# Performance work log

Hardware: AMD Instinct MI355X
Metric: run time of the kernel (lower is better)

## Reference

```python
import jax, jax.numpy as jnp
import numpy as np

B, T, U = 4, 256, 128
EH, PH, JH, V = 1024, 640, 640, 1024


def setup_inputs() -> dict:
    key = jax.random.key(0)
    ks = jax.random.split(key, 8)
    s_e = 1.0 / np.sqrt(EH)
    s_p = 1.0 / np.sqrt(PH)
    s_j = 1.0 / np.sqrt(JH)
    return {
        "enc": jax.random.normal(ks[0], (B, EH, T), jnp.float32),
        "dec": jax.random.normal(ks[1], (B, PH, U), jnp.float32),
        "W_enc": jax.random.uniform(ks[2], (JH, EH), jnp.float32, -s_e, s_e),
        "b_enc": jax.random.uniform(ks[3], (JH,), jnp.float32, -s_e, s_e),
        "W_pred": jax.random.uniform(ks[4], (JH, PH), jnp.float32, -s_p, s_p),
        "b_pred": jax.random.uniform(ks[5], (JH,), jnp.float32, -s_p, s_p),
        "W_out": jax.random.uniform(ks[6], (V, JH), jnp.float32, -s_j, s_j),
        "b_out": jax.random.uniform(ks[7], (V,), jnp.float32, -s_j, s_j),
    }


def reference(enc, dec, W_enc, b_enc, W_pred, b_pred, W_out, b_out):
    # enc: [B, EH, T], dec: [B, PH, U]  (channels-first, as in torch forward)
    # enc projection -> [B, T, JH] (transpose fused into einsum)
    e = jnp.einsum('bht,jh->btj', enc, W_enc) + b_enc
    # pred projection -> [B, U, JH]
    p = jnp.einsum('bhu,jh->buj', dec, W_pred) + b_pred
    # broadcast add -> [B, T, U, JH], ReLU, output projection -> [B, T, U, V]
    h = jax.nn.relu(e[:, :, None, :] + p[:, None, :, :])
    logits = jnp.einsum('btuj,vj->btuv', h, W_out) + b_out
    return jax.nn.log_softmax(logits, axis=-1)
```

## Files before the change

kernel.cpp:

```cpp
#include <hip/hip_runtime.h>
#include <hip/hip_bf16.h>
#include <stdint.h>

#define B_ 4
#define T_ 256
#define U_ 128
#define EH_ 1024
#define PH_ 640
#define JH_ 640
#define V_ 1024
#define KT_ 20

typedef short bf16x8 __attribute__((ext_vector_type(8)));
typedef float f32x4 __attribute__((ext_vector_type(4)));
typedef unsigned short u16;

__device__ __forceinline__ u16 f2bf(float f) {
  union { float f; uint32_t u; } v;
  v.f = f;
  uint32_t u = v.u;
  return (u16)((u + 0x7FFFu + ((u >> 16) & 1u)) >> 16);
}

__device__ __forceinline__ uint32_t cvt2(float lo, float hi) {
  uint32_t r;
  asm("v_cvt_pk_bf16_f32 %0, %1, %2" : "=v"(r) : "v"(lo), "v"(hi));
  return r;
}

#define LGKM0  asm volatile("s_waitcnt lgkmcnt(0)" ::: "memory")

__global__ void k_transpose_cvt(const float* __restrict__ in, u16* __restrict__ out,
                                int H, int W) {
  __shared__ float tile[32][33];
  int b = blockIdx.z;
  int h0 = blockIdx.y * 32, w0 = blockIdx.x * 32;
  const float* pin = in + (size_t)b * H * W;
  u16* pout = out + (size_t)b * H * W;
  int lw = threadIdx.x & 31, lh = threadIdx.x >> 5;
#pragma unroll
  for (int i = 0; i < 4; i++) {
    int h = lh + i * 8;
    tile[h][lw] = pin[(size_t)(h0 + h) * W + (w0 + lw)];
  }
  __syncthreads();
#pragma unroll
  for (int i = 0; i < 4; i++) {
    int w = lh + i * 8;
    pout[(size_t)(w0 + w) * H + (h0 + lw)] = f2bf(tile[lw][w]);
  }
}

__global__ void k_prep_w(const float* __restrict__ We, const float* __restrict__ Wp,
                         const float* __restrict__ Wo,
                         u16* __restrict__ WeB, u16* __restrict__ WpB,
                         u16* __restrict__ Wpk) {
  int s = blockIdx.x * 256 + threadIdx.x;
  if (s < 163840) {
    int idx = s * 4;
    float4 v = *(const float4*)(We + idx);
    ushort4 o;
    o.x = f2bf(v.x); o.y = f2bf(v.y); o.z = f2bf(v.z); o.w = f2bf(v.w);
    *(ushort4*)(WeB + idx) = o;
  } else if (s < 266240) {
    int idx = (s - 163840) * 4;
    float4 v = *(const float4*)(Wp + idx);
    ushort4 o;
    o.x = f2bf(v.x); o.y = f2bf(v.y); o.z = f2bf(v.z); o.w = f2bf(v.w);
    *(ushort4*)(WpB + idx) = o;
  } else {
    int q = s - 266240;
    int c = q & 1023;
    int g = (q >> 10) & 3;
    int t = q >> 12;
    const float* src = Wo + (size_t)c * JH_ + t * 32 + g * 8;
    float4 a = *(const float4*)src;
    float4 b2 = *(const float4*)(src + 4);
    ushort4 lo, hi;
    lo.x = f2bf(a.x);  lo.y = f2bf(a.y);  lo.z = f2bf(a.z);  lo.w = f2bf(a.w);
    hi.x = f2bf(b2.x); hi.y = f2bf(b2.y); hi.z = f2bf(b2.z); hi.w = f2bf(b2.w);
    u16* d = Wpk + (size_t)q * 8;
    *(ushort4*)d = lo;
    *(ushort4*)(d + 4) = hi;
  }
}

template<int PACK>
__global__ void k_proj_gemm(const u16* __restrict__ A, const u16* __restrict__ Bm,
                            const float* __restrict__ bias, float* __restrict__ C,
                            int K, int N, size_t strideA, size_t strideC) {
  __shared__ __align__(16) u16 sA[64 * 64];
  __shared__ __align__(16) u16 sB[64 * 64];
  int bb = blockIdx.z;
  const u16* Ab = A + (size_t)bb * strideA;
  float* Cb = C + (size_t)bb * strideC;
  int m0 = blockIdx.x * 64, n0 = blockIdx.y * 64;
  int tid = threadIdx.x;
  int lane = tid & 63, wid = tid >> 6;

  f32x4 acc[2][2] = {};
  for (int kk = 0; kk < K; kk += 64) {
#pragma unroll
    for (int i = 0; i < 2; i++) {
      int c = tid + i * 256;
      int r = c >> 3, kc = c & 7;
      int s = (r << 3) | (kc ^ (r & 7));
      *(bf16x8*)(sA + s * 8) = *(const bf16x8*)(Ab + (size_t)(m0 + r) * K + kk + kc * 8);
      *(bf16x8*)(sB + s * 8) = *(const bf16x8*)(Bm + (size_t)(n0 + r) * K + kk + kc * 8);
    }
    __syncthreads();
    int wr = (wid >> 1) * 32, wc = (wid & 1) * 32;
    int lr = lane & 15, lk = lane >> 4;
#pragma unroll
    for (int ki = 0; ki < 2; ki++) {
      bf16x8 af[2], bq[2];
#pragma unroll
      for (int mf = 0; mf < 2; mf++) {
        int r = wr + mf * 16 + lr;
        int kc = ki * 4 + lk;
        int s = (r << 3) | (kc ^ (r & 7));
        af[mf] = *(const bf16x8*)(sA + s * 8);
      }
#pragma unroll
      for (int nf = 0; nf < 2; nf++) {
        int r = wc + nf * 16 + lr;
        int kc = ki * 4 + lk;
        int s = (r << 3) | (kc ^ (r & 7));
        bq[nf] = *(const bf16x8*)(sB + s * 8);
      }
#pragma unroll
      for (int mf = 0; mf < 2; mf++)
#pragma unroll
        for (int nf = 0; nf < 2; nf++)
          acc[mf][nf] = __builtin_amdgcn_mfma_f32_16x16x32_bf16(af[mf], bq[nf], acc[mf][nf], 0, 0, 0);
    }
    __syncthreads();
  }
  int wr = (wid >> 1) * 32, wc = (wid & 1) * 32;
  int lr = lane & 15, lq = lane >> 4;
#pragma unroll
  for (int nf = 0; nf < 2; nf++) {
    int n = n0 + wc + nf * 16 + lr;
    float bv = bias[n];
#pragma unroll
    for (int mf = 0; mf < 2; mf++) {
#pragma unroll
      for (int r = 0; r < 4; r++) {
        int m = m0 + wr + mf * 16 + lq * 4 + r;
        float v = acc[mf][nf][r] + bv;
        if (PACK)
          Cb[(size_t)(m >> 6) * 40960 + (n >> 2) * 256 + (m & 63) * 4 + (n & 3)] = v;
        else
          Cb[(size_t)m * N + n] = v;
      }
    }
  }
}

__global__ __launch_bounds__(512)
void k_fused7(const float* __restrict__ e, const float* __restrict__ pPk,
              const u16* __restrict__ Wpk, const float* __restrict__ bout,
              float* __restrict__ out) {
  __shared__ __align__(16) u16 sA[2][4096];
  __shared__ __align__(16) float sE[JH_];
  __shared__ float redm[512];
  __shared__ float reds[512];

  int bid = blockIdx.x;
  int btile = bid >> 1, half = bid & 1, b = btile >> 8;
  int tid = threadIdx.x, lane = tid & 63, wn = tid >> 6;
  int lr = lane & 15, lk = lane >> 4;

  const float* eRow = e + (size_t)btile * JH_;
  const float* pPbase = pPk + ((size_t)(b * 2 + half) * 40960) + wn * 256 + lane * 4;
  const u16* wB = Wpk + ((size_t)lk * 1024 + wn * 128 + lr) * 8;
  float* outB = out + ((size_t)btile * U_ + half * 64) * V_;

  int awr = (wn >> 1) * 512 + lane * 8 + (wn & 1) * 4;

  f32x4 acc[4][8] = {};
  bf16x8 bq[2][8];

  auto loadB = [&](int t, bf16x8* d) {
#pragma unroll
    for (int nf = 0; nf < 8; nf++)
      d[nf] = *(const bf16x8*)(wB + (size_t)t * 32768 + nf * 128);
  };
  auto loadp = [&](int t) { return *(const float4*)(pPbase + t * 2048); };
  auto build = [&](int slot, int tin, int t, float4 pv) {
    float4 ev = *(const float4*)(&sE[t * 32 + wn * 4]);
    uint2 w;
    w.x = cvt2(fmaxf(pv.x + ev.x, 0.f), fmaxf(pv.y + ev.y, 0.f));
    w.y = cvt2(fmaxf(pv.z + ev.z, 0.f), fmaxf(pv.w + ev.w, 0.f));
    *(uint2*)(&sA[slot][tin * 2048 + awr]) = w;
  };

  loadB(0, bq[0]);
  for (int i = tid; i < JH_; i += 512) sE[i] = eRow[i];
  float4 p0  = loadp(0);
  float4 p1  = loadp(1);
  float4 pcA = loadp(2);
  float4 pcB = loadp(3);
  float4 pnA = p0, pnB = p0;
  LGKM0;
  __builtin_amdgcn_s_barrier();
  build(0, 0, 0, p0);
  build(0, 1, 1, p1);
  LGKM0;
  __builtin_amdgcn_s_barrier();

#pragma unroll
  for (int t = 0; t < KT_; t++) {
    if (t + 1 < KT_) loadB(t + 1, bq[(t + 1) & 1]);
    if ((t & 1) == 0) {
      if (t + 4 < KT_) { pnA = loadp(t + 4); pnB = loadp(t + 5); }
      if (t + 2 < KT_) {
        int q1 = ((t >> 1) + 1) & 1;
        build(q1, 0, t + 2, pcA);
        build(q1, 1, t + 3, pcB);
      }
    }
    const u16* Ab = &sA[(t >> 1) & 1][(t & 1) * 2048 + lk * 512];
    bf16x8 af[4];
#pragma unroll
    for (int mf = 0; mf < 4; mf++)
      af[mf] = *(const bf16x8*)(Ab + (mf * 16 + lr) * 8);
    __builtin_amdgcn_s_setprio(1);
#pragma unroll
    for (int mf = 0; mf < 4; mf++)
#pragma unroll
      for (int nf = 0; nf < 8; nf++)
        acc[mf][nf] = __builtin_amdgcn_mfma_f32_16x16x32_bf16(bq[t & 1][nf], af[mf], acc[mf][nf], 0, 0, 0);
    __builtin_amdgcn_s_setprio(0);
    if ((t & 1) && t + 1 < KT_) {
      pcA = pnA; pcB = pnB;
      LGKM0;
      __builtin_amdgcn_s_barrier();
    }
  }

#pragma unroll
  for (int nf = 0; nf < 8; nf++) {
    f32x4 bv = *(const f32x4*)(bout + wn * 128 + nf * 16 + lk * 4);
#pragma unroll
    for (int mf = 0; mf < 4; mf++) acc[mf][nf] += bv;
  }
  float gm[4], lsv[4];
#pragma unroll
  for (int mf = 0; mf < 4; mf++) {
    float m = acc[mf][0][0];
#pragma unroll
    for (int nf = 0; nf < 8; nf++)
#pragma unroll
      for (int j = 0; j < 4; j++) m = fmaxf(m, acc[mf][nf][j]);
    m = fmaxf(m, __shfl_xor(m, 16, 64));
    m = fmaxf(m, __shfl_xor(m, 32, 64));
    gm[mf] = m;
  }
  if (lane < 16) {
#pragma unroll
    for (int mf = 0; mf < 4; mf++) redm[(mf * 16 + lr) * 8 + wn] = gm[mf];
  }
  __syncthreads();
#pragma unroll
  for (int mf = 0; mf < 4; mf++) {
    float m = redm[(mf * 16 + lr) * 8];
#pragma unroll
    for (int w = 1; w < 8; w++) m = fmaxf(m, redm[(mf * 16 + lr) * 8 + w]);
    gm[mf] = m;
  }
#pragma unroll
  for (int mf = 0; mf < 4; mf++) {
    float s = 0.f;
#pragma unroll
    for (int nf = 0; nf < 8; nf++)
#pragma unroll
      for (int j = 0; j < 4; j++) s += __expf(acc[mf][nf][j] - gm[mf]);
    s += __shfl_xor(s, 16, 64);
    s += __shfl_xor(s, 32, 64);
    lsv[mf] = s;
  }
  if (lane < 16) {
#pragma unroll
    for (int mf = 0; mf < 4; mf++) reds[(mf * 16 + lr) * 8 + wn] = lsv[mf];
  }
  __syncthreads();
#pragma unroll
  for (int mf = 0; mf < 4; mf++) {
    float s = reds[(mf * 16 + lr) * 8];
#pragma unroll
    for (int w = 1; w < 8; w++) s += reds[(mf * 16 + lr) * 8 + w];
    lsv[mf] = gm[mf] + __logf(s);
  }

#pragma unroll
  for (int mf = 0; mf < 4; mf++) {
    float* orow = outB + (size_t)(mf * 16 + lr) * V_ + wn * 128 + lk * 4;
#pragma unroll
    for (int nf = 0; nf < 8; nf++) {
      f32x4 v = acc[mf][nf] - lsv[mf];
      *(f32x4*)(orow + nf * 16) = v;
    }
  }
}

extern "C" void kernel_launch(void* const* d_in, const int* in_sizes, int n_in,
                              void* d_out, int out_size, void* d_ws, size_t ws_size,
                              hipStream_t stream) {
  const float* enc    = (const float*)d_in[0];
  const float* dec    = (const float*)d_in[1];
  const float* W_enc  = (const float*)d_in[2];
  const float* b_enc  = (const float*)d_in[3];
  const float* W_pred = (const float*)d_in[4];
  const float* b_pred = (const float*)d_in[5];
  const float* W_out  = (const float*)d_in[6];
  const float* b_out  = (const float*)d_in[7];
  float* out = (float*)d_out;

  char* ws = (char*)d_ws;
  size_t off = 0;
  auto alloc = [&](size_t bytes) {
    void* pp = ws + off;
    off = (off + bytes + 255) & ~(size_t)255;
    return pp;
  };
  u16* encT   = (u16*)alloc((size_t)B_ * T_ * EH_ * 2);
  u16* decT   = (u16*)alloc((size_t)B_ * U_ * PH_ * 2);
  u16* WencB  = (u16*)alloc((size_t)JH_ * EH_ * 2);
  u16* WpredB = (u16*)alloc((size_t)JH_ * PH_ * 2);
  u16* Wpk    = (u16*)alloc((size_t)KT_ * 32768 * 2);
  float* eBuf = (float*)alloc((size_t)B_ * T_ * JH_ * 4);
  float* pPk  = (float*)alloc((size_t)81920 * 4 * 4);

  k_transpose_cvt<<<dim3(T_ / 32, EH_ / 32, B_), 256, 0, stream>>>(enc, encT, EH_, T_);
  k_transpose_cvt<<<dim3(U_ / 32, PH_ / 32, B_), 256, 0, stream>>>(dec, decT, PH_, U_);
  k_prep_w<<<1360, 256, 0, stream>>>(W_enc, W_pred, W_out, WencB, WpredB, Wpk);
  k_proj_gemm<0><<<dim3(T_ / 64, JH_ / 64, B_), 256, 0, stream>>>(
      encT, WencB, b_enc, eBuf, EH_, JH_, (size_t)T_ * EH_, (size_t)T_ * JH_);
  k_proj_gemm<1><<<dim3(U_ / 64, JH_ / 64, B_), 256, 0, stream>>>(
      decT, WpredB, b_pred, pPk, PH_, JH_, (size_t)U_ * PH_, (size_t)81920);

  k_fused7<<<B_ * T_ * 2, 512, 0, stream>>>(eBuf, pPk, Wpk, b_out, out);
}
```

Before: 276.0 us.

## Split fused joint kernel across 16 waves with narrower per-wave N tiles

Doubles the block to 1024 threads so each of 16 waves computes 64 vocabulary columns instead of 128. This halves the accumulator and B-fragment registers per wave and raises wave-level parallelism for latency hiding. Only the first 8 waves build the shared A tile, with the p-loads pipelined one stage shallower, and the softmax reductions widen to 16 waves. The cost is that each wave now reloads the A fragments for fewer MFMAs, and block-wide barriers cover more waves.

```diff
diff --git a/kernel.cpp b/kernel.cpp
--- a/kernel.cpp
+++ b/kernel.cpp
@@ -157,14 +157,14 @@
   }
 }
 
-__global__ __launch_bounds__(512)
-void k_fused7(const float* __restrict__ e, const float* __restrict__ pPk,
-              const u16* __restrict__ Wpk, const float* __restrict__ bout,
-              float* __restrict__ out) {
+__global__ __launch_bounds__(1024, 4)
+void k_fused10(const float* __restrict__ e, const float* __restrict__ pPk,
+               const u16* __restrict__ Wpk, const float* __restrict__ bout,
+               float* __restrict__ out) {
   __shared__ __align__(16) u16 sA[2][4096];
   __shared__ __align__(16) float sE[JH_];
-  __shared__ float redm[512];
-  __shared__ float reds[512];
+  __shared__ float redm[1024];
+  __shared__ float reds[1024];
 
   int bid = blockIdx.x;
   int btile = bid >> 1, half = bid & 1, b = btile >> 8;
@@ -172,23 +172,24 @@
   int lr = lane & 15, lk = lane >> 4;
 
   const float* eRow = e + (size_t)btile * JH_;
-  const float* pPbase = pPk + ((size_t)(b * 2 + half) * 40960) + wn * 256 + lane * 4;
-  const u16* wB = Wpk + ((size_t)lk * 1024 + wn * 128 + lr) * 8;
+  const u16* wB = Wpk + ((size_t)lk * 1024 + wn * 64 + lr) * 8;
   float* outB = out + ((size_t)btile * U_ + half * 64) * V_;
 
-  int awr = (wn >> 1) * 512 + lane * 8 + (wn & 1) * 4;
-
-  f32x4 acc[4][8] = {};
-  bf16x8 bq[2][8];
+  int awr = ((wn & 7) >> 1) * 512 + lane * 8 + (wn & 1) * 4;
+  const float* pPbase = pPk + ((size_t)(b * 2 + half) * 40960) + (wn & 7) * 256 + lane * 4;
+
+  f32x4 acc[4][4] = {};
+  bf16x8 bq[2][4];
+  float4 pA, pB;
 
   auto loadB = [&](int t, bf16x8* d) {
 #pragma unroll
-    for (int nf = 0; nf < 8; nf++)
+    for (int nf = 0; nf < 4; nf++)
       d[nf] = *(const bf16x8*)(wB + (size_t)t * 32768 + nf * 128);
   };
   auto loadp = [&](int t) { return *(const float4*)(pPbase + t * 2048); };
   auto build = [&](int slot, int tin, int t, float4 pv) {
-    float4 ev = *(const float4*)(&sE[t * 32 + wn * 4]);
+    float4 ev = *(const float4*)(&sE[t * 32 + (wn & 7) * 4]);
     uint2 w;
     w.x = cvt2(fmaxf(pv.x + ev.x, 0.f), fmaxf(pv.y + ev.y, 0.f));
     w.y = cvt2(fmaxf(pv.z + ev.z, 0.f), fmaxf(pv.w + ev.w, 0.f));
@@ -196,52 +197,46 @@
   };
 
   loadB(0, bq[0]);
-  for (int i = tid; i < JH_; i += 512) sE[i] = eRow[i];
-  float4 p0  = loadp(0);
-  float4 p1  = loadp(1);
-  float4 pcA = loadp(2);
-  float4 pcB = loadp(3);
-  float4 pnA = p0, pnB = p0;
+  for (int i = tid; i < JH_; i += 1024) sE[i] = eRow[i];
+  if (wn < 8) { pA = loadp(0); pB = loadp(1); }
   LGKM0;
   __builtin_amdgcn_s_barrier();
-  build(0, 0, 0, p0);
-  build(0, 1, 1, p1);
+  if (wn < 8) {
+    build(0, 0, 0, pA);
+    build(0, 1, 1, pB);
+    pA = loadp(2); pB = loadp(3);
+  }
   LGKM0;
   __builtin_amdgcn_s_barrier();
 
 #pragma unroll
   for (int t = 0; t < KT_; t++) {
     if (t + 1 < KT_) loadB(t + 1, bq[(t + 1) & 1]);
-    if ((t & 1) == 0) {
-      if (t + 4 < KT_) { pnA = loadp(t + 4); pnB = loadp(t + 5); }
-      if (t + 2 < KT_) {
-        int q1 = ((t >> 1) + 1) & 1;
-        build(q1, 0, t + 2, pcA);
-        build(q1, 1, t + 3, pcB);
-      }
+    if ((t & 1) && t + 1 < KT_ && wn < 8) {
+      int q1 = ((t >> 1) + 1) & 1;
+      build(q1, 0, t + 1, pA);
+      build(q1, 1, t + 2, pB);
+      if (t + 3 < KT_) { pA = loadp(t + 3); pB = loadp(t + 4); }
     }
     const u16* Ab = &sA[(t >> 1) & 1][(t & 1) * 2048 + lk * 512];
-    bf16x8 af[4];
-#pragma unroll
-    for (int mf = 0; mf < 4; mf++)
-      af[mf] = *(const bf16x8*)(Ab + (mf * 16 + lr) * 8);
-    __builtin_amdgcn_s_setprio(1);
-#pragma unroll
-    for (int mf = 0; mf < 4; mf++)
-#pragma unroll
-      for (int nf = 0; nf < 8; nf++)
-        acc[mf][nf] = __builtin_amdgcn_mfma_f32_16x16x32_bf16(bq[t & 1][nf], af[mf], acc[mf][nf], 0, 0, 0);
-    __builtin_amdgcn_s_setprio(0);
+#pragma unroll
+    for (int mf = 0; mf < 4; mf++) {
+      bf16x8 af = *(const bf16x8*)(Ab + (mf * 16 + lr) * 8);
+      __builtin_amdgcn_s_setprio(1);
+#pragma unroll
+      for (int nf = 0; nf < 4; nf++)
+        acc[mf][nf] = __builtin_amdgcn_mfma_f32_16x16x32_bf16(bq[t & 1][nf], af, acc[mf][nf], 0, 0, 0);
+      __builtin_amdgcn_s_setprio(0);
+    }
     if ((t & 1) && t + 1 < KT_) {
-      pcA = pnA; pcB = pnB;
       LGKM0;
       __builtin_amdgcn_s_barrier();
     }
   }
 
 #pragma unroll
-  for (int nf = 0; nf < 8; nf++) {
-    f32x4 bv = *(const f32x4*)(bout + wn * 128 + nf * 16 + lk * 4);
+  for (int nf = 0; nf < 4; nf++) {
+    f32x4 bv = *(const f32x4*)(bout + wn * 64 + nf * 16 + lk * 4);
 #pragma unroll
     for (int mf = 0; mf < 4; mf++) acc[mf][nf] += bv;
   }
@@ -250,7 +245,7 @@
   for (int mf = 0; mf < 4; mf++) {
     float m = acc[mf][0][0];
 #pragma unroll
-    for (int nf = 0; nf < 8; nf++)
+    for (int nf = 0; nf < 4; nf++)
 #pragma unroll
       for (int j = 0; j < 4; j++) m = fmaxf(m, acc[mf][nf][j]);
     m = fmaxf(m, __shfl_xor(m, 16, 64));
@@ -259,21 +254,21 @@
   }
   if (lane < 16) {
 #pragma unroll
-    for (int mf = 0; mf < 4; mf++) redm[(mf * 16 + lr) * 8 + wn] = gm[mf];
+    for (int mf = 0; mf < 4; mf++) redm[(mf * 16 + lr) * 16 + wn] = gm[mf];
   }
   __syncthreads();
 #pragma unroll
   for (int mf = 0; mf < 4; mf++) {
-    float m = redm[(mf * 16 + lr) * 8];
-#pragma unroll
-    for (int w = 1; w < 8; w++) m = fmaxf(m, redm[(mf * 16 + lr) * 8 + w]);
+    float m = redm[(mf * 16 + lr) * 16];
+#pragma unroll
+    for (int w = 1; w < 16; w++) m = fmaxf(m, redm[(mf * 16 + lr) * 16 + w]);
     gm[mf] = m;
   }
 #pragma unroll
   for (int mf = 0; mf < 4; mf++) {
     float s = 0.f;
 #pragma unroll
-    for (int nf = 0; nf < 8; nf++)
+    for (int nf = 0; nf < 4; nf++)
 #pragma unroll
       for (int j = 0; j < 4; j++) s += __expf(acc[mf][nf][j] - gm[mf]);
     s += __shfl_xor(s, 16, 64);
@@ -282,22 +277,22 @@
   }
   if (lane < 16) {
 #pragma unroll
-    for (int mf = 0; mf < 4; mf++) reds[(mf * 16 + lr) * 8 + wn] = lsv[mf];
+    for (int mf = 0; mf < 4; mf++) reds[(mf * 16 + lr) * 16 + wn] = lsv[mf];
   }
   __syncthreads();
 #pragma unroll
   for (int mf = 0; mf < 4; mf++) {
-    float s = reds[(mf * 16 + lr) * 8];
-#pragma unroll
-    for (int w = 1; w < 8; w++) s += reds[(mf * 16 + lr) * 8 + w];
+    float s = reds[(mf * 16 + lr) * 16];
+#pragma unroll
+    for (int w = 1; w < 16; w++) s += reds[(mf * 16 + lr) * 16 + w];
     lsv[mf] = gm[mf] + __logf(s);
   }
 
 #pragma unroll
   for (int mf = 0; mf < 4; mf++) {
-    float* orow = outB + (size_t)(mf * 16 + lr) * V_ + wn * 128 + lk * 4;
-#pragma unroll
-    for (int nf = 0; nf < 8; nf++) {
+    float* orow = outB + (size_t)(mf * 16 + lr) * V_ + wn * 64 + lk * 4;
+#pragma unroll
+    for (int nf = 0; nf < 4; nf++) {
       f32x4 v = acc[mf][nf] - lsv[mf];
       *(f32x4*)(orow + nf * 16) = v;
     }
@@ -340,5 +335,5 @@
   k_proj_gemm<1><<<dim3(U_ / 64, JH_ / 64, B_), 256, 0, stream>>>(
       decT, WpredB, b_pred, pPk, PH_, JH_, (size_t)U_ * PH_, (size_t)81920);
 
-  k_fused7<<<B_ * T_ * 2, 512, 0, stream>>>(eBuf, pPk, Wpk, b_out, out);
-}
+  k_fused10<<<B_ * T_ * 2, 1024, 0, stream>>>(eBuf, pPk, Wpk, b_out, out);
+}
```

Result: slower. 288.9 us (+4.7%).
